# Kernel optimization log

Measured on AMD Instinct MI355X. Metric: run time of the kernel, lower is better.

## Reference

```python
import jax, jax.numpy as jnp
import numpy as np

NUM_USERS = 40000
NUM_BUSINESSES = 60000
N = NUM_USERS + NUM_BUSINESSES
HIDDEN = 128
HEADS = 4
E = 200000
BATCH = 4096
NEG_SLOPE = 0.2  # PyG GATConv default


def setup_inputs() -> dict:
    key = jax.random.key(0)
    ks = jax.random.split(key, 20)
    s = 0.05
    inp = {
        "user_table": jax.random.normal(ks[0], (NUM_USERS, HIDDEN), jnp.float32) * s,
        "business_table": jax.random.normal(ks[1], (NUM_BUSINESSES, HIDDEN), jnp.float32) * s,
        # gat1: in=HIDDEN, out=HIDDEN, heads=HEADS
        "W1": jax.random.normal(ks[2], (HIDDEN, HEADS * HIDDEN), jnp.float32) * s,
        "att_src1": jax.random.normal(ks[3], (HEADS, HIDDEN), jnp.float32) * s,
        "att_dst1": jax.random.normal(ks[4], (HEADS, HIDDEN), jnp.float32) * s,
        "b1": jnp.zeros((HEADS * HIDDEN,), jnp.float32),
        # gat2: in=HEADS*HIDDEN, out=HIDDEN, heads=1
        "W2": jax.random.normal(ks[5], (HEADS * HIDDEN, HIDDEN), jnp.float32) * s,
        "att_src2": jax.random.normal(ks[6], (1, HIDDEN), jnp.float32) * s,
        "att_dst2": jax.random.normal(ks[7], (1, HIDDEN), jnp.float32) * s,
        "b2": jnp.zeros((HIDDEN,), jnp.float32),
        # predictor MLP
        "Wp1": jax.random.normal(ks[8], (2 * HIDDEN, HIDDEN), jnp.float32) * s,
        "bp1": jnp.zeros((HIDDEN,), jnp.float32),
        "Wp2": jax.random.normal(ks[9], (HIDDEN, 1), jnp.float32) * s,
        "bp2": jnp.zeros((1,), jnp.float32),
        "user_idx": jax.random.randint(ks[10], (BATCH,), 0, NUM_USERS),
        "business_idx": jax.random.randint(ks[11], (BATCH,), 0, NUM_BUSINESSES) + NUM_USERS,
        "edge_index": jax.random.randint(ks[12], (2, E), 0, N),
    }
    return inp


def gat_conv(x, edge_index, W, att_src, att_dst, bias, heads, out_ch, num_nodes):
    # add self-loops (PyG default add_self_loops=True)
    loop = jnp.arange(num_nodes)
    src = jnp.concatenate([edge_index[0], loop])
    dst = jnp.concatenate([edge_index[1], loop])
    h = (x @ W).reshape(num_nodes, heads, out_ch)            # [N,H,C]
    a_src = jnp.einsum('nhc,hc->nh', h, att_src)             # [N,H]
    a_dst = jnp.einsum('nhc,hc->nh', h, att_dst)             # [N,H]
    e = jax.nn.leaky_relu(a_src[src] + a_dst[dst], NEG_SLOPE)  # [E',H]
    # segment softmax over destination nodes
    emax = jax.ops.segment_max(e, dst, num_segments=num_nodes)
    emax = jnp.where(jnp.isfinite(emax), emax, 0.0)
    ex = jnp.exp(e - emax[dst])
    denom = jax.ops.segment_sum(ex, dst, num_segments=num_nodes)
    alpha = ex / (denom[dst] + 1e-16)                        # [E',H]
    msg = h[src] * alpha[..., None]                          # [E',H,C]
    out = jax.ops.segment_sum(msg, dst, num_segments=num_nodes)  # [N,H,C]
    return out.reshape(num_nodes, heads * out_ch) + bias


def reference(user_table, business_table, W1, att_src1, att_dst1, b1,
              W2, att_src2, att_dst2, b2, Wp1, bp1, Wp2, bp2,
              user_idx, business_idx, edge_index):
    user_emb = user_table[user_idx]                          # [B,HIDDEN]
    business_emb = business_table[business_idx - NUM_USERS]  # [B,HIDDEN]
    x = jnp.zeros((N, HIDDEN), jnp.float32)
    x = x.at[user_idx].set(user_emb)
    x = x.at[business_idx].set(business_emb)
    x = jax.nn.relu(gat_conv(x, edge_index, W1, att_src1, att_dst1, b1, HEADS, HIDDEN, N))
    x = gat_conv(x, edge_index, W2, att_src2, att_dst2, b2, 1, HIDDEN, N)
    feats = jnp.concatenate([x[user_idx], x[business_idx]], axis=1)  # [B,2*HIDDEN]
    hidden = jax.nn.relu(feats @ Wp1 + bp1)
    rating = hidden @ Wp2 + bp2                              # [B,1]
    return rating.squeeze(-1)
```

## Files before the change

### kernel.cpp

```cpp
#include <hip/hip_runtime.h>
#include <cstdint>
#include <cstddef>

#define NU      40000
#define NBZ     60000
#define NN      100000
#define HID     128
#define NHEADS  4
#define NE      200000
#define NBATCH  4096
#define BE      (2 * NBATCH)
#define SMAX    10240
#define CAP     16
#define SLOPE   0.2f

typedef __attribute__((ext_vector_type(8))) short short8v;
typedef __attribute__((ext_vector_type(4))) float f32x4;

__device__ __forceinline__ float lrelu(float x) { return x > 0.f ? x : SLOPE * x; }
__device__ __forceinline__ unsigned short f2bf(float f) {
  unsigned u = __float_as_uint(f);
  u += 0x7FFFu + ((u >> 16) & 1u);
  return (unsigned short)(u >> 16);
}


__global__ void k_init(int* __restrict__ node2slotB, int* __restrict__ flags,
                       int* __restrict__ cnt) {
  int i = blockIdx.x * blockDim.x + threadIdx.x;
  if (i < NN) { node2slotB[i] = 0; flags[i] = 0; }
  if (i == 0) *cnt = 0;
}

__global__ void k_mark(const int* __restrict__ user_idx, const int* __restrict__ business_idx,
                       int* __restrict__ node2slotB) {
  int i = blockIdx.x * blockDim.x + threadIdx.x;
  if (i >= BE) return;
  int node = (i < NBATCH) ? user_idx[i] : business_idx[i - NBATCH];
  node2slotB[node] = i + 1;
}

#define W1ATT_BLOCKS 64
#define WT_BLOCKS    640
__global__ __launch_bounds__(256)
void k_frontA(const float* __restrict__ W1, const float* __restrict__ W2,
              const float* __restrict__ Wp1,
              const float* __restrict__ att_src1, const float* __restrict__ att_dst1,
              float* __restrict__ wsrc, float* __restrict__ wdst,
              short* __restrict__ w1t, short* __restrict__ w2t, short* __restrict__ wp1t,
              const int* __restrict__ ei, const int* __restrict__ n2sB,
              int* __restrict__ flags) {
  int bid = blockIdx.x, tid = threadIdx.x;
  if (bid >= W1ATT_BLOCKS + WT_BLOCKS) {
    int e = (bid - W1ATT_BLOCKS - WT_BLOCKS) * 256 + tid;
    if (e < NE) {
      int s = ei[e], d = ei[NE + e];
      if (n2sB[d] > 0) atomicOr(&flags[s], 2);
      if (n2sB[s] > 0) atomicOr(&flags[d], 1);
    }
    return;
  }
  if (bid >= W1ATT_BLOCKS) {
    int t = (bid - W1ATT_BLOCKS) * 256 + tid;
    if (t < 65536) {
      int c = t >> 14, kn = t & 16383, k = kn >> 7, n = kn & 127;
      w1t[c * 16384 + n * 128 + k] = (short)f2bf(W1[(size_t)k * 512 + c * 128 + n]);
    } else if (t < 131072) {
      int t2 = t - 65536;
      int c = t2 >> 14, kn = t2 & 16383, k = kn >> 7, n = kn & 127;
      w2t[c * 16384 + n * 128 + k] = (short)f2bf(W2[(size_t)(c * 128 + k) * 128 + n]);
    } else if (t < 163840) {
      int t3 = t - 131072;
      int k = t3 >> 7, n = t3 & 127;
      wp1t[n * 256 + k] = (short)f2bf(Wp1[(size_t)k * HID + n]);
    }
    return;
  }
  __shared__ float red[2][2][8];
  int kk = tid >> 7, c = tid & 127;
  int k = bid * 2 + kk;
  float ps[4], pd[4];
#pragma unroll
  for (int h = 0; h < 4; ++h) {
    float wv = W1[(size_t)k * 512 + h * 128 + c];
    ps[h] = wv * att_src1[h * 128 + c];
    pd[h] = wv * att_dst1[h * 128 + c];
  }
#pragma unroll
  for (int off = 1; off < 64; off <<= 1) {
#pragma unroll
    for (int h = 0; h < 4; ++h) { ps[h] += __shfl_xor(ps[h], off); pd[h] += __shfl_xor(pd[h], off); }
  }
  int half = (tid >> 6) & 1;
  if ((tid & 63) == 0) {
#pragma unroll
    for (int h = 0; h < 4; ++h) { red[kk][half][h] = ps[h]; red[kk][half][h + 4] = pd[h]; }
  }
  __syncthreads();
  if ((tid & 127) == 0) {
#pragma unroll
    for (int h = 0; h < 4; ++h) {
      wsrc[k * 4 + h] = red[kk][0][h] + red[kk][1][h];
      wdst[k * 4 + h] = red[kk][0][h + 4] + red[kk][1][h + 4];
    }
  }
}

#define SCAL1_BLOCKS (BE / 4)
__global__ __launch_bounds__(256)
void k_mid(const float* __restrict__ user_table, const float* __restrict__ business_table,
           const int* __restrict__ user_idx, const int* __restrict__ business_idx,
           const float* __restrict__ wsrc, const float* __restrict__ wdst,
           float* __restrict__ a_src1c, float* __restrict__ a_dst1c,
           const int* __restrict__ n2sB, const int* __restrict__ flags,
           int* __restrict__ slotN, int* __restrict__ slot2node, int* __restrict__ cnt,
           int* __restrict__ fillc1, int* __restrict__ indegS,
           int* __restrict__ fillc2, int* __restrict__ indegB) {
  int bid = blockIdx.x, tid = threadIdx.x;
  if (bid >= SCAL1_BLOCKS) {
    int v = (bid - SCAL1_BLOCKS) * 256 + tid;
    if (v >= NN) return;
    if (v < SMAX) { fillc1[v] = 0; indegS[v] = 0; }
    if (v < BE)   { fillc2[v] = 0; indegB[v] = 0; }
    bool need = (n2sB[v] > 0) || ((flags[v] & 3) == 3);
    int s = -1;
    if (need) {
      s = atomicAdd(cnt, 1);
      if (s >= SMAX) s = -1;
      else slot2node[s] = v;
    }
    slotN[v] = s;
    return;
  }
  int w = bid * 4 + (tid >> 6);
  int lane = tid & 63;
  int node = (w < NBATCH) ? user_idx[w] : business_idx[w - NBATCH];
  const float* src = (w < NBATCH) ? (user_table + (size_t)node * HID)
                                  : (business_table + (size_t)(node - NU) * HID);
  float2 e = *(const float2*)(src + lane * 2);
  float4 w0s = *(const float4*)(wsrc + (lane * 2) * 4);
  float4 w1s = *(const float4*)(wsrc + (lane * 2 + 1) * 4);
  float4 w0d = *(const float4*)(wdst + (lane * 2) * 4);
  float4 w1d = *(const float4*)(wdst + (lane * 2 + 1) * 4);
  float ss[4] = {e.x * w0s.x + e.y * w1s.x, e.x * w0s.y + e.y * w1s.y,
                 e.x * w0s.z + e.y * w1s.z, e.x * w0s.w + e.y * w1s.w};
  float dd[4] = {e.x * w0d.x + e.y * w1d.x, e.x * w0d.y + e.y * w1d.y,
                 e.x * w0d.z + e.y * w1d.z, e.x * w0d.w + e.y * w1d.w};
#pragma unroll
  for (int off = 1; off < 64; off <<= 1) {
#pragma unroll
    for (int h = 0; h < 4; ++h) { ss[h] += __shfl_xor(ss[h], off); dd[h] += __shfl_xor(dd[h], off); }
  }
  if (lane == 0) {
    float4 o1 = {ss[0], ss[1], ss[2], ss[3]};
    float4 o2 = {dd[0], dd[1], dd[2], dd[3]};
    *(float4*)(a_src1c + w * 4) = o1;
    *(float4*)(a_dst1c + w * 4) = o2;
  }
}

__global__ void k_fillb(const int* __restrict__ ei, const int* __restrict__ n2sB,
                        const int* __restrict__ slotN,
                        int* __restrict__ fillc1, int* __restrict__ indegS, int* __restrict__ list1,
                        int* __restrict__ fillc2, int* __restrict__ indegB, int* __restrict__ list2) {
  int e = blockIdx.x * blockDim.x + threadIdx.x;
  if (e >= NE) return;
  int s = ei[e], d = ei[NE + e];
  int snd = slotN[d];
  if (snd >= 0) {
    atomicAdd(&indegS[snd], 1);
    int sBr = n2sB[s];
    if (sBr > 0) { int p = atomicAdd(&fillc1[snd], 1); if (p < CAP) list1[snd * CAP + p] = sBr - 1; }
  }
  int dBr = n2sB[d];
  if (dBr > 0) {
    int dB = dBr - 1;
    atomicAdd(&indegB[dB], 1);
    int sns = slotN[s];
    if (sns >= 0) { int p = atomicAdd(&fillc2[dB], 1); if (p < CAP) list2[dB * CAP + p] = sns; }
  }
}

__global__ __launch_bounds__(256)
void k_agg1emb(const int* __restrict__ slot2node, const int* __restrict__ n2sB,
               const int* __restrict__ indegS, const int* __restrict__ fillc1,
               const int* __restrict__ list1,
               const float* __restrict__ a_src1c, const float* __restrict__ a_dst1c,
               const float* __restrict__ user_table, const float* __restrict__ business_table,
               const int* __restrict__ user_idx, const int* __restrict__ business_idx,
               const int* __restrict__ cntp, short* __restrict__ eaggb) {
  int w = (blockIdx.x * blockDim.x + threadIdx.x) >> 6;
  int lane = threadIdx.x & 63;
  int M = *cntp; if (M > SMAX) M = SMAX;
  if (w >= M) return;
  int v = slot2node[w];
  int dB = n2sB[v] - 1;
  float ad[4] = {0.f, 0.f, 0.f, 0.f};
  if (dB >= 0) {
    float4 a = *(const float4*)(a_dst1c + dB * 4);
    ad[0] = a.x; ad[1] = a.y; ad[2] = a.z; ad[3] = a.w;
  }
  int ne = fillc1[w];
  int nnb = indegS[w] + 1 - ne - (dB >= 0 ? 1 : 0);
  float m[4], sum[4], ax[4], ay[4];
#pragma unroll
  for (int h = 0; h < 4; ++h) {
    if (nnb > 0) { m[h] = lrelu(ad[h]); sum[h] = (float)nnb; }
    else { m[h] = -3.0e38f; sum[h] = 0.f; }
    ax[h] = 0.f; ay[h] = 0.f;
  }
  for (int j = (dB >= 0 ? -1 : 0); j < ne; ++j) {
    int sB = (j < 0) ? dB : list1[w * CAP + j];
    float4 as4 = *(const float4*)(a_src1c + sB * 4);
    float as[4] = {as4.x, as4.y, as4.z, as4.w};
    int node = (sB < NBATCH) ? user_idx[sB] : business_idx[sB - NBATCH];
    const float* src = (sB < NBATCH) ? (user_table + (size_t)node * HID)
                                     : (business_table + (size_t)(node - NU) * HID);
    float2 e = *(const float2*)(src + lane * 2);
#pragma unroll
    for (int h = 0; h < 4; ++h) {
      float x = lrelu(as[h] + ad[h]);
      if (x > m[h]) {
        float r = __expf(m[h] - x);
        sum[h] = sum[h] * r + 1.f;
        ax[h] = ax[h] * r + e.x;
        ay[h] = ay[h] * r + e.y;
        m[h] = x;
      } else {
        float p = __expf(x - m[h]);
        sum[h] += p;
        ax[h] += p * e.x;
        ay[h] += p * e.y;
      }
    }
  }
  unsigned short* o = (unsigned short*)eaggb + (size_t)w * 512;
#pragma unroll
  for (int h = 0; h < 4; ++h) {
    float r = 1.f / (sum[h] + 1e-16f);
    unsigned lo = f2bf(ax[h] * r), hi = f2bf(ay[h] * r);
    *(unsigned*)(o + h * 128 + lane * 2) = lo | (hi << 16);
  }
}

__global__ __launch_bounds__(256)
void k_mm01(const short* __restrict__ A, const short* __restrict__ W1t,
            const short* __restrict__ W2t, const float* __restrict__ bias,
            const int* __restrict__ cntp, float* __restrict__ part) {
  __shared__ unsigned short Tl[64][132];
  int M = *cntp; if (M > SMAX) M = SMAX;
  int row0 = blockIdx.x * 64;
  if (row0 >= M) return;
  int c = blockIdx.y;
  int lane = threadIdx.x & 63;
  int wid = threadIdx.x >> 6;
  int l15 = lane & 15, g = lane >> 4;
  int kq = g * 8;
  f32x4 acc[4][2];
#pragma unroll
  for (int i = 0; i < 4; ++i)
#pragma unroll
    for (int j = 0; j < 2; ++j) acc[i][j] = (f32x4){0.f, 0.f, 0.f, 0.f};
#pragma unroll
  for (int k0 = 0; k0 < 128; k0 += 32) {
    short8v av[4], bv[2];
#pragma unroll
    for (int i = 0; i < 4; ++i) {
      int rA = row0 + i * 16 + l15; if (rA >= M) rA = M - 1;
      av[i] = *(const short8v*)(A + (size_t)rA * 512 + c * 128 + k0 + kq);
    }
#pragma unroll
    for (int j = 0; j < 2; ++j) {
      int col = wid * 32 + j * 16 + l15;
      bv[j] = *(const short8v*)(W1t + ((size_t)c * 128 + col) * 128 + k0 + kq);
    }
#pragma unroll
    for (int i = 0; i < 4; ++i)
#pragma unroll
      for (int j = 0; j < 2; ++j)
        acc[i][j] = __builtin_amdgcn_mfma_f32_16x16x32_bf16(av[i], bv[j], acc[i][j], 0, 0, 0);
  }
#pragma unroll
  for (int j = 0; j < 2; ++j) {
    int col = wid * 32 + j * 16 + l15;
    float bvv = bias[c * 128 + col];
#pragma unroll
    for (int i = 0; i < 4; ++i) {
#pragma unroll
      for (int q = 0; q < 4; ++q) {
        int r = i * 16 + g * 4 + q;
        Tl[r][col] = f2bf(fmaxf(acc[i][j][q] + bvv, 0.f));
      }
    }
  }
  __syncthreads();
#pragma unroll
  for (int i = 0; i < 4; ++i)
#pragma unroll
    for (int j = 0; j < 2; ++j) acc[i][j] = (f32x4){0.f, 0.f, 0.f, 0.f};
#pragma unroll
  for (int k0 = 0; k0 < 128; k0 += 32) {
    short8v av[4], bv[2];
#pragma unroll
    for (int i = 0; i < 4; ++i)
      av[i] = *(const short8v*)&Tl[i * 16 + l15][k0 + kq];
#pragma unroll
    for (int j = 0; j < 2; ++j) {
      int col = wid * 32 + j * 16 + l15;
      bv[j] = *(const short8v*)(W2t + ((size_t)c * 128 + col) * 128 + k0 + kq);
    }
#pragma unroll
    for (int i = 0; i < 4; ++i)
#pragma unroll
      for (int j = 0; j < 2; ++j)
        acc[i][j] = __builtin_amdgcn_mfma_f32_16x16x32_bf16(av[i], bv[j], acc[i][j], 0, 0, 0);
  }
  float* Cp = part + (size_t)c * SMAX * HID;
#pragma unroll
  for (int j = 0; j < 2; ++j) {
    int col = wid * 32 + j * 16 + l15;
#pragma unroll
    for (int i = 0; i < 4; ++i) {
#pragma unroll
      for (int q = 0; q < 4; ++q) {
        int r = row0 + i * 16 + g * 4 + q;
        if (r < M) Cp[(size_t)r * HID + col] = acc[i][j][q];
      }
    }
  }
}

__global__ __launch_bounds__(256)
void k_agg2h(const int* __restrict__ user_idx, const int* __restrict__ business_idx,
             const int* __restrict__ n2sB, const int* __restrict__ slotN,
             const int* __restrict__ indegB, const int* __restrict__ fillc2,
             const int* __restrict__ list2, const float* __restrict__ part,
             const float* __restrict__ att_src2, const float* __restrict__ att_dst2,
             const float* __restrict__ b2, short* __restrict__ x2b) {
  int w = (blockIdx.x * blockDim.x + threadIdx.x) >> 6;
  int lane = threadIdx.x & 63;
  if (w >= BE) return;
  int node = (w < NBATCH) ? user_idx[w] : business_idx[w - NBATCH];
  if (n2sB[node] != w + 1) return;
  int snd = slotN[node];
  int c0 = lane * 2;
  float as2a = att_src2[c0], as2b = att_src2[c0 + 1];
  float ad2a = att_dst2[c0], ad2b = att_dst2[c0 + 1];
  size_t offS = (size_t)snd * HID + c0;
  float2 q0 = *(const float2*)(part + offS);
  float2 q1 = *(const float2*)(part + (size_t)SMAX * HID + offS);
  float2 q2 = *(const float2*)(part + (size_t)2 * SMAX * HID + offS);
  float2 q3 = *(const float2*)(part + (size_t)3 * SMAX * HID + offS);
  float hs0 = (q0.x + q1.x) + (q2.x + q3.x);
  float hs1 = (q0.y + q1.y) + (q2.y + q3.y);
  float ssS = hs0 * as2a + hs1 * as2b;
  float adS = hs0 * ad2a + hs1 * ad2b;
#pragma unroll
  for (int off = 1; off < 64; off <<= 1) { ssS += __shfl_xor(ssS, off); adS += __shfl_xor(adS, off); }
  float ad = adS;
  int ne = fillc2[w];
  int nnb = indegB[w] - ne;
  float m, sum;
  if (nnb > 0) { m = lrelu(ad); sum = (float)nnb; } else { m = -3.0e38f; sum = 0.f; }
  float a0 = 0.f, a1 = 0.f;
  {
    float x = lrelu(ssS + ad);
    if (x > m) { float r = __expf(m - x); sum = sum * r + 1.f; a0 = a0 * r + hs0; a1 = a1 * r + hs1; m = x; }
    else { float p = __expf(x - m); sum += p; a0 += p * hs0; a1 += p * hs1; }
  }
  for (int j = 0; j < ne; ++j) {
    int sn = list2[w * CAP + j];
    size_t off2 = (size_t)sn * HID + c0;
    float2 p0 = *(const float2*)(part + off2);
    float2 p1 = *(const float2*)(part + (size_t)SMAX * HID + off2);
    float2 p2 = *(const float2*)(part + (size_t)2 * SMAX * HID + off2);
    float2 p3 = *(const float2*)(part + (size_t)3 * SMAX * HID + off2);
    float r0 = (p0.x + p1.x) + (p2.x + p3.x);
    float r1 = (p0.y + p1.y) + (p2.y + p3.y);
    float ss = r0 * as2a + r1 * as2b;
#pragma unroll
    for (int off = 1; off < 64; off <<= 1) ss += __shfl_xor(ss, off);
    float x = lrelu(ss + ad);
    if (x > m) { float r = __expf(m - x); sum = sum * r + 1.f; a0 = a0 * r + r0; a1 = a1 * r + r1; m = x; }
    else { float p = __expf(x - m); sum += p; a0 += p * r0; a1 += p * r1; }
  }
  float r = 1.f / (sum + 1e-16f);
  unsigned lo = f2bf(a0 * r + b2[c0]);
  unsigned hi = f2bf(a1 * r + b2[c0 + 1]);
  *(unsigned*)((unsigned short*)x2b + (size_t)w * HID + c0) = lo | (hi << 16);
}

__global__ __launch_bounds__(512)
void k_mlp(const short* __restrict__ x2b, const short* __restrict__ wp1t,
           const int* __restrict__ user_idx, const int* __restrict__ business_idx,
           const int* __restrict__ n2sB,
           const float* __restrict__ bp1, const float* __restrict__ Wp2,
           const float* __restrict__ bp2, float* __restrict__ out) {
  __shared__ float pout[8][16];
  int row0 = blockIdx.x * 16;
  int lane = threadIdx.x & 63;
  int w = threadIdx.x >> 6;
  int l15 = lane & 15, g = lane >> 4;
  int kq = g * 8;
  int p = row0 + l15;
  int us = n2sB[user_idx[p]] - 1;
  int bs = n2sB[business_idx[p]] - 1;
  int nn = w * 16 + l15;
  f32x4 acc = {0.f, 0.f, 0.f, 0.f};
  const short* bpw = wp1t + (size_t)nn * 256 + kq;
#pragma unroll
  for (int k0 = 0; k0 < 256; k0 += 32) {
    int slot = (k0 < 128) ? us : bs;
    short8v a = *(const short8v*)(x2b + (size_t)slot * HID + (k0 & 127) + kq);
    short8v b = *(const short8v*)(bpw + k0);
    acc = __builtin_amdgcn_mfma_f32_16x16x32_bf16(a, b, acc, 0, 0, 0);
  }
  float bpv = bp1[nn], wpv = Wp2[nn];
#pragma unroll
  for (int j = 0; j < 4; ++j) {
    float v = fmaxf(acc[j] + bpv, 0.f) * wpv;
#pragma unroll
    for (int off = 1; off < 16; off <<= 1) v += __shfl_xor(v, off);
    if (l15 == 0) pout[w][g * 4 + j] = v;
  }
  __syncthreads();
  int tid = threadIdx.x;
  if (tid < 16) {
    float s = 0.f;
#pragma unroll
    for (int q = 0; q < 8; ++q) s += pout[q][tid];
    out[row0 + tid] = s + bp2[0];
  }
}

extern "C" void kernel_launch(void* const* d_in, const int* in_sizes, int n_in,
                              void* d_out, int out_size, void* d_ws, size_t ws_size,
                              hipStream_t stream) {
  const float* user_table     = (const float*)d_in[0];
  const float* business_table = (const float*)d_in[1];
  const float* W1       = (const float*)d_in[2];
  const float* att_src1 = (const float*)d_in[3];
  const float* att_dst1 = (const float*)d_in[4];
  const float* b1       = (const float*)d_in[5];
  const float* W2       = (const float*)d_in[6];
  const float* att_src2 = (const float*)d_in[7];
  const float* att_dst2 = (const float*)d_in[8];
  const float* b2       = (const float*)d_in[9];
  const float* Wp1      = (const float*)d_in[10];
  const float* bp1      = (const float*)d_in[11];
  const float* Wp2      = (const float*)d_in[12];
  const float* bp2      = (const float*)d_in[13];
  const int* user_idx     = (const int*)d_in[14];
  const int* business_idx = (const int*)d_in[15];
  const int* ei           = (const int*)d_in[16];
  float* out = (float*)d_out;

  char* w = (char*)d_ws;
  size_t used = 0;
  auto alloc = [&](size_t bytes) -> void* {
    void* p = w + used;
    used += (bytes + 255) & ~(size_t)255;
    return p;
  };
  int*   node2slotB = (int*)alloc((size_t)NN * 4);
  int*   flags      = (int*)alloc((size_t)NN * 4);
  int*   slotN      = (int*)alloc((size_t)NN * 4);
  int*   slot2node  = (int*)alloc((size_t)SMAX * 4);
  int*   cnt        = (int*)alloc(256);
  float* wsrc       = (float*)alloc((size_t)HID * 4 * 4);
  float* wdst       = (float*)alloc((size_t)HID * 4 * 4);
  float* a_src1c    = (float*)alloc((size_t)BE * 4 * 4);
  float* a_dst1c    = (float*)alloc((size_t)BE * 4 * 4);
  int*   fillc1     = (int*)alloc((size_t)SMAX * 4);
  int*   indegS     = (int*)alloc((size_t)SMAX * 4);
  int*   list1      = (int*)alloc((size_t)SMAX * CAP * 4);
  int*   fillc2     = (int*)alloc((size_t)BE * 4);
  int*   indegB     = (int*)alloc((size_t)BE * 4);
  int*   list2      = (int*)alloc((size_t)BE * CAP * 4);
  short* w1t        = (short*)alloc((size_t)NHEADS * HID * HID * 2);
  short* w2t        = (short*)alloc((size_t)NHEADS * HID * HID * 2);
  short* wp1t       = (short*)alloc((size_t)HID * 256 * 2);
  short* eaggb      = (short*)alloc((size_t)SMAX * 512 * 2);
  float* part       = (float*)alloc((size_t)NHEADS * SMAX * HID * 4);
  short* x2b        = (short*)alloc((size_t)BE * HID * 2);
  if (used > ws_size) return;

  const int T = 256;
  auto cdiv = [](int a, int b) { return (a + b - 1) / b; };

  k_init<<<cdiv(NN, T), T, 0, stream>>>(node2slotB, flags, cnt);
  k_mark<<<cdiv(BE, T), T, 0, stream>>>(user_idx, business_idx, node2slotB);

  k_frontA<<<W1ATT_BLOCKS + WT_BLOCKS + cdiv(NE, T), T, 0, stream>>>(
      W1, W2, Wp1, att_src1, att_dst1, wsrc, wdst, w1t, w2t, wp1t,
      ei, node2slotB, flags);

  k_mid<<<SCAL1_BLOCKS + cdiv(NN, T), T, 0, stream>>>(
      user_table, business_table, user_idx, business_idx, wsrc, wdst,
      a_src1c, a_dst1c, node2slotB, flags, slotN, slot2node, cnt,
      fillc1, indegS, fillc2, indegB);

  k_fillb<<<cdiv(NE, T), T, 0, stream>>>(ei, node2slotB, slotN,
                                         fillc1, indegS, list1, fillc2, indegB, list2);

  k_agg1emb<<<cdiv(SMAX * 64, T), T, 0, stream>>>(
      slot2node, node2slotB, indegS, fillc1, list1, a_src1c, a_dst1c,
      user_table, business_table, user_idx, business_idx, cnt, eaggb);

  k_mm01<<<dim3(SMAX / 64, NHEADS), T, 0, stream>>>(eaggb, w1t, w2t, b1, cnt, part);

  k_agg2h<<<cdiv(BE * 64, T), T, 0, stream>>>(user_idx, business_idx, node2slotB, slotN,
                                              indegB, fillc2, list2, part,
                                              att_src2, att_dst2, b2, x2b);

  k_mlp<<<NBATCH / 16, 512, 0, stream>>>(x2b, wp1t, user_idx, business_idx, node2slotB,
                                         bp1, Wp2, bp2, out);
}
```

Baseline: 85.73 us.

## Fuse head loop in GEMM kernel and precompute layer-2 attention scalars

The second-layer GEMM kernel now loops over all four heads inside one block, accumulating the layer-2 projection in registers instead of writing four per-head partial sums to global memory. It also computes the per-row attention source and destination scalars in the epilogue, so the aggregation kernel reads one h2 row plus two scalars per neighbour instead of four partials plus a 64-lane reduction. This cuts global traffic and per-edge shuffles, at the cost of a grid four times smaller with a serial head loop per block, which lowers parallelism in the GEMM.

Result: slower. 92.02 us (+7.3%).

```diff
diff --git a/kernel.cpp b/kernel.cpp
--- a/kernel.cpp
+++ b/kernel.cpp
@@ -246,87 +246,111 @@
 __global__ __launch_bounds__(256)
 void k_mm01(const short* __restrict__ A, const short* __restrict__ W1t,
             const short* __restrict__ W2t, const float* __restrict__ bias,
-            const int* __restrict__ cntp, float* __restrict__ part) {
+            const float* __restrict__ att_src2, const float* __restrict__ att_dst2,
+            const int* __restrict__ cntp, float* __restrict__ h2c,
+            float* __restrict__ a_src2c, float* __restrict__ a_dst2c) {
   __shared__ unsigned short Tl[64][132];
+  __shared__ float pss[4][64], pdd[4][64];
   int M = *cntp; if (M > SMAX) M = SMAX;
   int row0 = blockIdx.x * 64;
   if (row0 >= M) return;
-  int c = blockIdx.y;
   int lane = threadIdx.x & 63;
   int wid = threadIdx.x >> 6;
   int l15 = lane & 15, g = lane >> 4;
   int kq = g * 8;
-  f32x4 acc[4][2];
+  f32x4 h2acc[4][2];
 #pragma unroll
   for (int i = 0; i < 4; ++i)
 #pragma unroll
-    for (int j = 0; j < 2; ++j) acc[i][j] = (f32x4){0.f, 0.f, 0.f, 0.f};
-#pragma unroll
-  for (int k0 = 0; k0 < 128; k0 += 32) {
-    short8v av[4], bv[2];
-#pragma unroll
-    for (int i = 0; i < 4; ++i) {
-      int rA = row0 + i * 16 + l15; if (rA >= M) rA = M - 1;
-      av[i] = *(const short8v*)(A + (size_t)rA * 512 + c * 128 + k0 + kq);
-    }
+    for (int j = 0; j < 2; ++j) h2acc[i][j] = (f32x4){0.f, 0.f, 0.f, 0.f};
+
+  for (int c = 0; c < NHEADS; ++c) {
+    f32x4 acc[4][2];
+#pragma unroll
+    for (int i = 0; i < 4; ++i)
+#pragma unroll
+      for (int j = 0; j < 2; ++j) acc[i][j] = (f32x4){0.f, 0.f, 0.f, 0.f};
+#pragma unroll
+    for (int k0 = 0; k0 < 128; k0 += 32) {
+      short8v av[4], bv[2];
+#pragma unroll
+      for (int i = 0; i < 4; ++i) {
+        int rA = row0 + i * 16 + l15; if (rA >= M) rA = M - 1;
+        av[i] = *(const short8v*)(A + (size_t)rA * 512 + c * 128 + k0 + kq);
+      }
+#pragma unroll
+      for (int j = 0; j < 2; ++j) {
+        int col = wid * 32 + j * 16 + l15;
+        bv[j] = *(const short8v*)(W1t + ((size_t)c * 128 + col) * 128 + k0 + kq);
+      }
+#pragma unroll
+      for (int i = 0; i < 4; ++i)
+#pragma unroll
+        for (int j = 0; j < 2; ++j)
+          acc[i][j] = __builtin_amdgcn_mfma_f32_16x16x32_bf16(av[i], bv[j], acc[i][j], 0, 0, 0);
+    }
+    __syncthreads();
 #pragma unroll
     for (int j = 0; j < 2; ++j) {
       int col = wid * 32 + j * 16 + l15;
-      bv[j] = *(const short8v*)(W1t + ((size_t)c * 128 + col) * 128 + k0 + kq);
-    }
-#pragma unroll
-    for (int i = 0; i < 4; ++i)
-#pragma unroll
-      for (int j = 0; j < 2; ++j)
-        acc[i][j] = __builtin_amdgcn_mfma_f32_16x16x32_bf16(av[i], bv[j], acc[i][j], 0, 0, 0);
-  }
+      float bvv = bias[c * 128 + col];
+#pragma unroll
+      for (int i = 0; i < 4; ++i) {
+#pragma unroll
+        for (int q = 0; q < 4; ++q)
+          Tl[i * 16 + g * 4 + q][col] = f2bf(fmaxf(acc[i][j][q] + bvv, 0.f));
+      }
+    }
+    __syncthreads();
+#pragma unroll
+    for (int k0 = 0; k0 < 128; k0 += 32) {
+      short8v av[4], bv[2];
+#pragma unroll
+      for (int i = 0; i < 4; ++i)
+        av[i] = *(const short8v*)&Tl[i * 16 + l15][k0 + kq];
+#pragma unroll
+      for (int j = 0; j < 2; ++j) {
+        int col = wid * 32 + j * 16 + l15;
+        bv[j] = *(const short8v*)(W2t + ((size_t)c * 128 + col) * 128 + k0 + kq);
+      }
+#pragma unroll
+      for (int i = 0; i < 4; ++i)
+#pragma unroll
+        for (int j = 0; j < 2; ++j)
+          h2acc[i][j] = __builtin_amdgcn_mfma_f32_16x16x32_bf16(av[i], bv[j], h2acc[i][j], 0, 0, 0);
+    }
+  }
+  float as2[2], ad2[2];
 #pragma unroll
   for (int j = 0; j < 2; ++j) {
     int col = wid * 32 + j * 16 + l15;
-    float bvv = bias[c * 128 + col];
-#pragma unroll
-    for (int i = 0; i < 4; ++i) {
-#pragma unroll
-      for (int q = 0; q < 4; ++q) {
-        int r = i * 16 + g * 4 + q;
-        Tl[r][col] = f2bf(fmaxf(acc[i][j][q] + bvv, 0.f));
+    as2[j] = att_src2[col];
+    ad2[j] = att_dst2[col];
+  }
+#pragma unroll
+  for (int i = 0; i < 4; ++i) {
+#pragma unroll
+    for (int q = 0; q < 4; ++q) {
+      int rl = i * 16 + g * 4 + q;
+      int r = row0 + rl;
+      float vs = 0.f, vd = 0.f;
+#pragma unroll
+      for (int j = 0; j < 2; ++j) {
+        float v = h2acc[i][j][q];
+        if (r < M) h2c[(size_t)r * HID + wid * 32 + j * 16 + l15] = v;
+        vs += v * as2[j];
+        vd += v * ad2[j];
       }
+#pragma unroll
+      for (int off = 1; off < 16; off <<= 1) { vs += __shfl_xor(vs, off); vd += __shfl_xor(vd, off); }
+      if (l15 == 0) { pss[wid][rl] = vs; pdd[wid][rl] = vd; }
     }
   }
   __syncthreads();
-#pragma unroll
-  for (int i = 0; i < 4; ++i)
-#pragma unroll
-    for (int j = 0; j < 2; ++j) acc[i][j] = (f32x4){0.f, 0.f, 0.f, 0.f};
-#pragma unroll
-  for (int k0 = 0; k0 < 128; k0 += 32) {
-    short8v av[4], bv[2];
-#pragma unroll
-    for (int i = 0; i < 4; ++i)
-      av[i] = *(const short8v*)&Tl[i * 16 + l15][k0 + kq];
-#pragma unroll
-    for (int j = 0; j < 2; ++j) {
-      int col = wid * 32 + j * 16 + l15;
-      bv[j] = *(const short8v*)(W2t + ((size_t)c * 128 + col) * 128 + k0 + kq);
-    }
-#pragma unroll
-    for (int i = 0; i < 4; ++i)
-#pragma unroll
-      for (int j = 0; j < 2; ++j)
-        acc[i][j] = __builtin_amdgcn_mfma_f32_16x16x32_bf16(av[i], bv[j], acc[i][j], 0, 0, 0);
-  }
-  float* Cp = part + (size_t)c * SMAX * HID;
-#pragma unroll
-  for (int j = 0; j < 2; ++j) {
-    int col = wid * 32 + j * 16 + l15;
-#pragma unroll
-    for (int i = 0; i < 4; ++i) {
-#pragma unroll
-      for (int q = 0; q < 4; ++q) {
-        int r = row0 + i * 16 + g * 4 + q;
-        if (r < M) Cp[(size_t)r * HID + col] = acc[i][j][q];
-      }
-    }
+  int tid = threadIdx.x;
+  if (tid < 64 && row0 + tid < M) {
+    a_src2c[row0 + tid] = (pss[0][tid] + pss[1][tid]) + (pss[2][tid] + pss[3][tid]);
+    a_dst2c[row0 + tid] = (pdd[0][tid] + pdd[1][tid]) + (pdd[2][tid] + pdd[3][tid]);
   }
 }
 
@@ -334,8 +358,8 @@
 void k_agg2h(const int* __restrict__ user_idx, const int* __restrict__ business_idx,
              const int* __restrict__ n2sB, const int* __restrict__ slotN,
              const int* __restrict__ indegB, const int* __restrict__ fillc2,
-             const int* __restrict__ list2, const float* __restrict__ part,
-             const float* __restrict__ att_src2, const float* __restrict__ att_dst2,
+             const int* __restrict__ list2, const float* __restrict__ h2c,
+             const float* __restrict__ a_src2c, const float* __restrict__ a_dst2c,
              const float* __restrict__ b2, short* __restrict__ x2b) {
   int w = (blockIdx.x * blockDim.x + threadIdx.x) >> 6;
   int lane = threadIdx.x & 63;
@@ -343,48 +367,31 @@
   int node = (w < NBATCH) ? user_idx[w] : business_idx[w - NBATCH];
   if (n2sB[node] != w + 1) return;
   int snd = slotN[node];
-  int c0 = lane * 2;
-  float as2a = att_src2[c0], as2b = att_src2[c0 + 1];
-  float ad2a = att_dst2[c0], ad2b = att_dst2[c0 + 1];
-  size_t offS = (size_t)snd * HID + c0;
-  float2 q0 = *(const float2*)(part + offS);
-  float2 q1 = *(const float2*)(part + (size_t)SMAX * HID + offS);
-  float2 q2 = *(const float2*)(part + (size_t)2 * SMAX * HID + offS);
-  float2 q3 = *(const float2*)(part + (size_t)3 * SMAX * HID + offS);
-  float hs0 = (q0.x + q1.x) + (q2.x + q3.x);
-  float hs1 = (q0.y + q1.y) + (q2.y + q3.y);
-  float ssS = hs0 * as2a + hs1 * as2b;
-  float adS = hs0 * ad2a + hs1 * ad2b;
-#pragma unroll
-  for (int off = 1; off < 64; off <<= 1) { ssS += __shfl_xor(ssS, off); adS += __shfl_xor(adS, off); }
-  float ad = adS;
+  float ad = a_dst2c[snd];
   int ne = fillc2[w];
   int nnb = indegB[w] - ne;
   float m, sum;
   if (nnb > 0) { m = lrelu(ad); sum = (float)nnb; } else { m = -3.0e38f; sum = 0.f; }
   float a0 = 0.f, a1 = 0.f;
-  {
-    float x = lrelu(ssS + ad);
-    if (x > m) { float r = __expf(m - x); sum = sum * r + 1.f; a0 = a0 * r + hs0; a1 = a1 * r + hs1; m = x; }
-    else { float p = __expf(x - m); sum += p; a0 += p * hs0; a1 += p * hs1; }
-  }
-  for (int j = 0; j < ne; ++j) {
-    int sn = list2[w * CAP + j];
-    size_t off2 = (size_t)sn * HID + c0;
-    float2 p0 = *(const float2*)(part + off2);
-    float2 p1 = *(const float2*)(part + (size_t)SMAX * HID + off2);
-    float2 p2 = *(const float2*)(part + (size_t)2 * SMAX * HID + off2);
-    float2 p3 = *(const float2*)(part + (size_t)3 * SMAX * HID + off2);
-    float r0 = (p0.x + p1.x) + (p2.x + p3.x);
-    float r1 = (p0.y + p1.y) + (p2.y + p3.y);
-    float ss = r0 * as2a + r1 * as2b;
-#pragma unroll
-    for (int off = 1; off < 64; off <<= 1) ss += __shfl_xor(ss, off);
-    float x = lrelu(ss + ad);
-    if (x > m) { float r = __expf(m - x); sum = sum * r + 1.f; a0 = a0 * r + r0; a1 = a1 * r + r1; m = x; }
-    else { float p = __expf(x - m); sum += p; a0 += p * r0; a1 += p * r1; }
+  for (int j = -1; j < ne; ++j) {
+    int sn = (j < 0) ? snd : list2[w * CAP + j];
+    float x = lrelu(a_src2c[sn] + ad);
+    float2 hv = *(const float2*)(h2c + (size_t)sn * HID + lane * 2);
+    if (x > m) {
+      float r = __expf(m - x);
+      sum = sum * r + 1.f;
+      a0 = a0 * r + hv.x;
+      a1 = a1 * r + hv.y;
+      m = x;
+    } else {
+      float p = __expf(x - m);
+      sum += p;
+      a0 += p * hv.x;
+      a1 += p * hv.y;
+    }
   }
   float r = 1.f / (sum + 1e-16f);
+  int c0 = lane * 2;
   unsigned lo = f2bf(a0 * r + b2[c0]);
   unsigned hi = f2bf(a1 * r + b2[c0 + 1]);
   *(unsigned*)((unsigned short*)x2b + (size_t)w * HID + c0) = lo | (hi << 16);
@@ -481,7 +488,9 @@
   short* w2t        = (short*)alloc((size_t)NHEADS * HID * HID * 2);
   short* wp1t       = (short*)alloc((size_t)HID * 256 * 2);
   short* eaggb      = (short*)alloc((size_t)SMAX * 512 * 2);
-  float* part       = (float*)alloc((size_t)NHEADS * SMAX * HID * 4);
+  float* h2c        = (float*)alloc((size_t)SMAX * HID * 4);
+  float* a_src2c    = (float*)alloc((size_t)SMAX * 4);
+  float* a_dst2c    = (float*)alloc((size_t)SMAX * 4);
   short* x2b        = (short*)alloc((size_t)BE * HID * 2);
   if (used > ws_size) return;
 
@@ -507,11 +516,12 @@
       slot2node, node2slotB, indegS, fillc1, list1, a_src1c, a_dst1c,
       user_table, business_table, user_idx, business_idx, cnt, eaggb);
 
-  k_mm01<<<dim3(SMAX / 64, NHEADS), T, 0, stream>>>(eaggb, w1t, w2t, b1, cnt, part);
+  k_mm01<<<SMAX / 64, T, 0, stream>>>(eaggb, w1t, w2t, b1, att_src2, att_dst2,
+                                      cnt, h2c, a_src2c, a_dst2c);
 
   k_agg2h<<<cdiv(BE * 64, T), T, 0, stream>>>(user_idx, business_idx, node2slotB, slotN,
-                                              indegB, fillc2, list2, part,
-                                              att_src2, att_dst2, b2, x2b);
+                                              indegB, fillc2, list2, h2c,
+                                              a_src2c, a_dst2c, b2, x2b);
 
   k_mlp<<<NBATCH / 16, 512, 0, stream>>>(x2b, wp1t, user_idx, business_idx, node2slotB,
                                          bp1, Wp2, bp2, out);
```
